# Kernel optimization log

Measured on AMD Instinct MI355X. Metric: run time of the kernel, lower is better.

The kernel has to match this reference:

```python
import jax, jax.numpy as jnp
import numpy as np

DIM = 512        # token feature dim
HID = 1024       # expert hidden dim (dim * 2)
E = 16           # num_experts
N = 8192         # num tokens
TOPK = 2         # experts active per token (routing sparsity)


def setup_inputs() -> dict:
    key = jax.random.key(0)
    k_x, k_s, k_w1, k_w2 = jax.random.split(key, 4)
    x = jax.random.normal(k_x, (N, DIM), dtype=jnp.float32)
    # sparse routing scores: top-2 experts per token get nonzero score, rest 0
    scores = jax.random.uniform(k_s, (N, E), dtype=jnp.float32)
    vals, idx = jax.lax.top_k(scores, TOPK)
    routing_tensor = jnp.zeros((N, E), jnp.float32).at[jnp.arange(N)[:, None], idx].set(vals)
    # per-expert MLP params (depth=2, bias=True): Linear(DIM->HID), GELU, Linear(HID->DIM)
    W1 = jax.random.normal(k_w1, (E, DIM, HID), dtype=jnp.float32) * (1.0 / np.sqrt(DIM))
    b1 = jnp.zeros((E, HID), jnp.float32)
    W2 = jax.random.normal(k_w2, (E, HID, DIM), dtype=jnp.float32) * (1.0 / np.sqrt(HID))
    b2 = jnp.zeros((E, DIM), jnp.float32)
    return {"x": x, "routing_tensor": routing_tensor, "W1": W1, "b1": b1, "W2": W2, "b2": b2}


def reference(x, routing_tensor, W1, b1, W2, b2):
    # out[n] = sum_e routing[n,e] * MLP_e(x[n]); rows with score 0 contribute 0,
    # which is exactly the original mask-gather / scatter-add semantics.
    h = jax.nn.gelu(jnp.einsum('nd,edh->enh', x, W1) + b1[:, None, :], approximate=False)
    y = jnp.einsum('enh,ehd->end', h, W2) + b2[:, None, :]  # [E, N, DIM]
    return jnp.einsum('end,ne->nd', y, routing_tensor)       # combine weighted by scores
```

## Files before the change

kernel.cpp:

```cpp
#include <hip/hip_runtime.h>
#include <hip/hip_bf16.h>

#define NTOK 8192
#define DIM 512
#define HID 1024
#define NE 16
#define CAP 1280
#define MT 20

typedef __attribute__((ext_vector_type(8))) short short8;
typedef __attribute__((ext_vector_type(4))) float f32x4;

static __device__ __forceinline__ unsigned short f2bf(float f) {
    __hip_bfloat16 h = __float2bfloat16(f);
    return __builtin_bit_cast(unsigned short, h);
}

static __device__ __forceinline__ void gl_lds16(const unsigned short* g, unsigned short* l) {
    __builtin_amdgcn_global_load_lds(
        (const __attribute__((address_space(1))) unsigned int*)g,
        (__attribute__((address_space(3))) unsigned int*)l, 16, 0, 0);
}

static __device__ __forceinline__ float gelu_f(float v) {
    float u = v * (0.7978845608f + 0.0356774081f * v * v);
    return v / (1.0f + __expf(-2.0f * u));
}

__global__ void transpose_cvt2(const float* __restrict__ W1, const float* __restrict__ W2,
                               unsigned short* __restrict__ w1t, unsigned short* __restrict__ w2t) {
    __shared__ float tile[32][33];
    int b = blockIdx.x;
    const float* src; unsigned short* dst; int R, C, bx, by;
    if (b < 8192) {
        int e = b >> 9, rem = b & 511; bx = rem & 31; by = rem >> 5;
        R = DIM; C = HID;
        src = W1 + (size_t)e * R * C; dst = w1t + (size_t)e * R * C;
    } else {
        int bb = b - 8192;
        int e = bb >> 9, rem = bb & 511; bx = rem & 15; by = rem >> 4;
        R = HID; C = DIM;
        src = W2 + (size_t)e * R * C; dst = w2t + (size_t)e * R * C;
    }
    int c0 = bx * 32, r0 = by * 32;
    int tx = threadIdx.x, ty = threadIdx.y;
    #pragma unroll
    for (int i = 0; i < 32; i += 8)
        tile[ty + i][tx] = src[(size_t)(r0 + ty + i) * C + c0 + tx];
    __syncthreads();
    #pragma unroll
    for (int i = 0; i < 32; i += 8)
        dst[(size_t)(c0 + ty + i) * R + r0 + tx] = f2bf(tile[tx][ty + i]);
}

__global__ __launch_bounds__(256) void route_fill(const float* __restrict__ routing,
                                                  int* __restrict__ cnt,
                                                  int* __restrict__ sidx,
                                                  float* __restrict__ wtb) {
    __shared__ int lcnt[NE], lbase[NE];
    int t = threadIdx.x;
    int n = blockIdx.x * 256 + t;
    if (t < NE) lcnt[t] = 0;
    __syncthreads();
    int mye[2]; float myw[2]; int mypos[2]; int slot = 0;
    #pragma unroll
    for (int e = 0; e < NE; e++) {
        float r = routing[n * NE + e];
        if (r != 0.0f && slot < 2) {
            mye[slot] = e; myw[slot] = r;
            mypos[slot] = atomicAdd(&lcnt[e], 1);
            slot++;
        }
    }
    __syncthreads();
    if (t < NE) lbase[t] = atomicAdd(&cnt[t], lcnt[t]);
    __syncthreads();
    for (int s = 0; s < slot; s++) {
        int e = mye[s];
        int p = lbase[e] + mypos[s];
        if (p < CAP) { sidx[e * CAP + p] = n * 2 + s; wtb[e * CAP + p] = myw[s]; }
    }
}

__global__ void gather_x(const float* __restrict__ x, const int* __restrict__ cnt,
                         const int* __restrict__ sidx, unsigned short* __restrict__ xg) {
    int b = blockIdx.x;
    int e = b / CAP, row = b - e * CAP;
    int t = threadIdx.x;
    int c = cnt[e]; c = c > CAP ? CAP : c;
    ushort4 o;
    if (row < c) {
        int n = sidx[b] >> 1;
        float4 v = ((const float4*)(x + (size_t)n * DIM))[t];
        o.x = f2bf(v.x); o.y = f2bf(v.y); o.z = f2bf(v.z); o.w = f2bf(v.w);
    } else {
        o.x = 0; o.y = 0; o.z = 0; o.w = 0;
    }
    ((ushort4*)(xg + (size_t)b * DIM))[t] = o;
}

template <int K>
__device__ __forceinline__ void mfma_main64(const unsigned short* __restrict__ A,
                                            const unsigned short* __restrict__ B,
                                            unsigned short* As, unsigned short* Bs,
                                            f32x4 acc[2][4]) {
    int t = threadIdx.x;
    int wave = t >> 6, lane = t & 63;
    int wm = wave >> 1, wn = wave & 1;
    int quad = lane >> 4, l16 = lane & 15;
    int lr = lane >> 3;
    int col = (lane & 7) << 3;
    for (int kc = 0; kc < K; kc += 64) {
        __syncthreads();
        #pragma unroll
        for (int j = 0; j < 2; j++) {
            int rb = wave * 16 + j * 8;
            gl_lds16(A + (size_t)(rb + lr) * K + kc + col, As + rb * 64);
        }
        #pragma unroll
        for (int j = 0; j < 4; j++) {
            int rb = wave * 32 + j * 8;
            gl_lds16(B + (size_t)(rb + lr) * K + kc + col, Bs + rb * 64);
        }
        __syncthreads();
        #pragma unroll
        for (int kk = 0; kk < 64; kk += 32) {
            short8 av[2], bv[4];
            #pragma unroll
            for (int mt = 0; mt < 2; mt++)
                av[mt] = *(const short8*)(&As[(wm * 32 + mt * 16 + l16) * 64 + kk + quad * 8]);
            #pragma unroll
            for (int nt = 0; nt < 4; nt++)
                bv[nt] = *(const short8*)(&Bs[(wn * 64 + nt * 16 + l16) * 64 + kk + quad * 8]);
            #pragma unroll
            for (int mt = 0; mt < 2; mt++)
                #pragma unroll
                for (int nt = 0; nt < 4; nt++)
                    acc[mt][nt] = __builtin_amdgcn_mfma_f32_16x16x32_bf16(
                        av[mt], bv[nt], acc[mt][nt], 0, 0, 0);
        }
    }
}


__global__ __launch_bounds__(256, 5) void gemm1_gelu(
    const unsigned short* __restrict__ xg, const unsigned short* __restrict__ w1t,
    const float* __restrict__ b1, const int* __restrict__ cnt,
    unsigned short* __restrict__ hbuf) {
    __shared__ __align__(16) unsigned short As[64 * 64];
    __shared__ __align__(16) unsigned short Bs[128 * 64];
    int L = blockIdx.x;
    int cc = L & 7, n = (L >> 3) & 7, g = L >> 6;
    int pi = cc + (g << 3);
    int e = pi / MT, m = pi % MT;
    int c = cnt[e]; c = c > CAP ? CAP : c;
    int m0 = m * 64;
    if (m0 >= c) return;
    int n0 = n * 128;
    const unsigned short* A = xg + ((size_t)e * CAP + m0) * DIM;
    const unsigned short* B = w1t + ((size_t)e * HID + n0) * DIM;
    f32x4 z = {0.f, 0.f, 0.f, 0.f};
    f32x4 acc[2][4];
    #pragma unroll
    for (int mt = 0; mt < 2; mt++)
        #pragma unroll
        for (int nt = 0; nt < 4; nt++) acc[mt][nt] = z;
    mfma_main64<DIM>(A, B, As, Bs, acc);
    int t = threadIdx.x;
    int wave = t >> 6, lane = t & 63;
    int wm = wave >> 1, wn = wave & 1, quad = lane >> 4, l16 = lane & 15;
    #pragma unroll
    for (int nt = 0; nt < 4; nt++) {
        int gn = n0 + wn * 64 + nt * 16 + l16;
        float bias = b1[e * HID + gn];
        #pragma unroll
        for (int mt = 0; mt < 2; mt++) {
            #pragma unroll
            for (int r = 0; r < 4; r++) {
                int gm = m0 + wm * 32 + mt * 16 + quad * 4 + r;
                float v = acc[mt][nt][r] + bias;
                hbuf[((size_t)e * CAP + gm) * HID + gn] = f2bf(gelu_f(v));
            }
        }
    }
}

__global__ __launch_bounds__(256, 5) void gemm2_store(
    const unsigned short* __restrict__ hbuf, const unsigned short* __restrict__ w2t,
    const float* __restrict__ b2, const int* __restrict__ cnt,
    const int* __restrict__ sidx, const float* __restrict__ wtb,
    float* __restrict__ ybuf) {
    __shared__ __align__(16) unsigned short As[64 * 64];
    __shared__ __align__(16) unsigned short Bs[128 * 64];
    int L = blockIdx.x;
    int cc = L & 7, n = (L >> 3) & 3, g = L >> 5;
    int pi = cc + (g << 3);
    int e = pi / MT, m = pi % MT;
    int c = cnt[e]; c = c > CAP ? CAP : c;
    int m0 = m * 64;
    if (m0 >= c) return;
    int n0 = n * 128;
    const unsigned short* A = hbuf + ((size_t)e * CAP + m0) * HID;
    const unsigned short* B = w2t + ((size_t)e * DIM + n0) * HID;
    f32x4 z = {0.f, 0.f, 0.f, 0.f};
    f32x4 acc[2][4];
    #pragma unroll
    for (int mt = 0; mt < 2; mt++)
        #pragma unroll
        for (int nt = 0; nt < 4; nt++) acc[mt][nt] = z;
    mfma_main64<HID>(A, B, As, Bs, acc);
    int t = threadIdx.x;
    int wave = t >> 6, lane = t & 63;
    int wm = wave >> 1, wn = wave & 1, quad = lane >> 4, l16 = lane & 15;
    #pragma unroll
    for (int mt = 0; mt < 2; mt++) {
        #pragma unroll
        for (int r = 0; r < 4; r++) {
            int gm = m0 + wm * 32 + mt * 16 + quad * 4 + r;
            if (gm < c) {
                int si = sidx[e * CAP + gm];
                float wgt = wtb[e * CAP + gm];
                float* yrow = ybuf + (size_t)si * DIM;
                #pragma unroll
                for (int nt = 0; nt < 4; nt++) {
                    int gn = n0 + wn * 64 + nt * 16 + l16;
                    yrow[gn] = wgt * (acc[mt][nt][r] + b2[e * DIM + gn]);
                }
            }
        }
    }
}

__global__ void combine(const float* __restrict__ yb, float* __restrict__ out) {
    int i = blockIdx.x * 256 + threadIdx.x;
    int n = i >> 7, d4 = i & 127;
    float4 a = ((const float4*)(yb + (size_t)(2 * n) * DIM))[d4];
    float4 b = ((const float4*)(yb + (size_t)(2 * n + 1) * DIM))[d4];
    float4 o;
    o.x = a.x + b.x; o.y = a.y + b.y; o.z = a.z + b.z; o.w = a.w + b.w;
    ((float4*)(out + (size_t)n * DIM))[d4] = o;
}

extern "C" void kernel_launch(void* const* d_in, const int* in_sizes, int n_in,
                              void* d_out, int out_size, void* d_ws, size_t ws_size,
                              hipStream_t stream) {
    const float* x       = (const float*)d_in[0];
    const float* routing = (const float*)d_in[1];
    const float* W1      = (const float*)d_in[2];
    const float* b1      = (const float*)d_in[3];
    const float* W2      = (const float*)d_in[4];
    const float* b2      = (const float*)d_in[5];
    float* out = (float*)d_out;

    char* w = (char*)d_ws;
    int*   cnt  = (int*)w;
    int*   sidx = (int*)(w + 256);
    float* wtb  = (float*)(w + 256 + NE * CAP * 4);
    char* base = w + 256 + NE * CAP * 8;
    unsigned short* xg  = (unsigned short*)base;
    unsigned short* hb  = xg + (size_t)NE * CAP * DIM;
    unsigned short* w1t = hb + (size_t)NE * CAP * HID;
    unsigned short* w2t = w1t + (size_t)NE * HID * DIM;
    float* ybuf = (float*)(w2t + (size_t)NE * DIM * HID);

    hipMemsetAsync(cnt, 0, 256, stream);

    transpose_cvt2<<<16384, dim3(32, 8), 0, stream>>>(W1, W2, w1t, w2t);

    route_fill<<<NTOK / 256, 256, 0, stream>>>(routing, cnt, sidx, wtb);
    gather_x<<<NE * CAP, 128, 0, stream>>>(x, cnt, sidx, xg);

    gemm1_gelu<<<8 * MT * NE, 256, 0, stream>>>(xg, w1t, b1, cnt, hb);
    gemm2_store<<<4 * MT * NE, 256, 0, stream>>>(hb, w2t, b2, cnt, sidx, wtb, ybuf);
    combine<<<(NTOK * DIM / 4) / 256, 256, 0, stream>>>(ybuf, out);
}
```

Baseline: 226.8 us.

## Merge weight transpose with routing, remap GEMM blocks so each XCD owns experts

Fuses the weight transpose/convert kernel and the routing-fill kernel into one launch, removing a kernel launch boundary. Remaps GEMM block indices so each XCD processes whole experts (expert = xcd + 8*half), so that expert's weights stay resident in that XCD's L2 cache. Raises the launch-bounds occupancy hint from 5 to 6 waves per SIMD for both GEMMs, which may force register limits or spills.

```diff
diff --git a/kernel.cpp b/kernel.cpp
--- a/kernel.cpp
+++ b/kernel.cpp
@@ -27,58 +27,61 @@
     return v / (1.0f + __expf(-2.0f * u));
 }
 
-__global__ void transpose_cvt2(const float* __restrict__ W1, const float* __restrict__ W2,
-                               unsigned short* __restrict__ w1t, unsigned short* __restrict__ w2t) {
-    __shared__ float tile[32][33];
+__global__ __launch_bounds__(256) void prep(const float* __restrict__ W1,
+                                            const float* __restrict__ W2,
+                                            unsigned short* __restrict__ w1t,
+                                            unsigned short* __restrict__ w2t,
+                                            const float* __restrict__ routing,
+                                            int* __restrict__ cnt,
+                                            int* __restrict__ sidx,
+                                            float* __restrict__ wtb) {
     int b = blockIdx.x;
-    const float* src; unsigned short* dst; int R, C, bx, by;
-    if (b < 8192) {
-        int e = b >> 9, rem = b & 511; bx = rem & 31; by = rem >> 5;
-        R = DIM; C = HID;
-        src = W1 + (size_t)e * R * C; dst = w1t + (size_t)e * R * C;
+    int t = threadIdx.x;
+    if (b < 16384) {
+        __shared__ float tile[32][33];
+        const float* src; unsigned short* dst; int R, C, bx, by;
+        if (b < 8192) {
+            int e = b >> 9, rem = b & 511; bx = rem & 31; by = rem >> 5;
+            R = DIM; C = HID;
+            src = W1 + (size_t)e * R * C; dst = w1t + (size_t)e * R * C;
+        } else {
+            int bb = b - 8192;
+            int e = bb >> 9, rem = bb & 511; bx = rem & 15; by = rem >> 4;
+            R = HID; C = DIM;
+            src = W2 + (size_t)e * R * C; dst = w2t + (size_t)e * R * C;
+        }
+        int c0 = bx * 32, r0 = by * 32;
+        int tx = t & 31, ty = t >> 5;
+        #pragma unroll
+        for (int i = 0; i < 32; i += 8)
+            tile[ty + i][tx] = src[(size_t)(r0 + ty + i) * C + c0 + tx];
+        __syncthreads();
+        #pragma unroll
+        for (int i = 0; i < 32; i += 8)
+            dst[(size_t)(c0 + ty + i) * R + r0 + tx] = f2bf(tile[tx][ty + i]);
     } else {
-        int bb = b - 8192;
-        int e = bb >> 9, rem = bb & 511; bx = rem & 15; by = rem >> 4;
-        R = HID; C = DIM;
-        src = W2 + (size_t)e * R * C; dst = w2t + (size_t)e * R * C;
-    }
-    int c0 = bx * 32, r0 = by * 32;
-    int tx = threadIdx.x, ty = threadIdx.y;
-    #pragma unroll
-    for (int i = 0; i < 32; i += 8)
-        tile[ty + i][tx] = src[(size_t)(r0 + ty + i) * C + c0 + tx];
-    __syncthreads();
-    #pragma unroll
-    for (int i = 0; i < 32; i += 8)
-        dst[(size_t)(c0 + ty + i) * R + r0 + tx] = f2bf(tile[tx][ty + i]);
-}
-
-__global__ __launch_bounds__(256) void route_fill(const float* __restrict__ routing,
-                                                  int* __restrict__ cnt,
-                                                  int* __restrict__ sidx,
-                                                  float* __restrict__ wtb) {
-    __shared__ int lcnt[NE], lbase[NE];
-    int t = threadIdx.x;
-    int n = blockIdx.x * 256 + t;
-    if (t < NE) lcnt[t] = 0;
-    __syncthreads();
-    int mye[2]; float myw[2]; int mypos[2]; int slot = 0;
-    #pragma unroll
-    for (int e = 0; e < NE; e++) {
-        float r = routing[n * NE + e];
-        if (r != 0.0f && slot < 2) {
-            mye[slot] = e; myw[slot] = r;
-            mypos[slot] = atomicAdd(&lcnt[e], 1);
-            slot++;
-        }
-    }
-    __syncthreads();
-    if (t < NE) lbase[t] = atomicAdd(&cnt[t], lcnt[t]);
-    __syncthreads();
-    for (int s = 0; s < slot; s++) {
-        int e = mye[s];
-        int p = lbase[e] + mypos[s];
-        if (p < CAP) { sidx[e * CAP + p] = n * 2 + s; wtb[e * CAP + p] = myw[s]; }
+        __shared__ int lcnt[NE], lbase[NE];
+        int n = (b - 16384) * 256 + t;
+        if (t < NE) lcnt[t] = 0;
+        __syncthreads();
+        int mye[2]; float myw[2]; int mypos[2]; int slot = 0;
+        #pragma unroll
+        for (int e = 0; e < NE; e++) {
+            float r = routing[n * NE + e];
+            if (r != 0.0f && slot < 2) {
+                mye[slot] = e; myw[slot] = r;
+                mypos[slot] = atomicAdd(&lcnt[e], 1);
+                slot++;
+            }
+        }
+        __syncthreads();
+        if (t < NE) lbase[t] = atomicAdd(&cnt[t], lcnt[t]);
+        __syncthreads();
+        for (int s = 0; s < slot; s++) {
+            int e = mye[s];
+            int p = lbase[e] + mypos[s];
+            if (p < CAP) { sidx[e * CAP + p] = n * 2 + s; wtb[e * CAP + p] = myw[s]; }
+        }
     }
 }
 
@@ -143,16 +146,18 @@
 }
 
 
-__global__ __launch_bounds__(256, 5) void gemm1_gelu(
+__global__ __launch_bounds__(256, 6) void gemm1_gelu(
     const unsigned short* __restrict__ xg, const unsigned short* __restrict__ w1t,
     const float* __restrict__ b1, const int* __restrict__ cnt,
     unsigned short* __restrict__ hbuf) {
     __shared__ __align__(16) unsigned short As[64 * 64];
     __shared__ __align__(16) unsigned short Bs[128 * 64];
     int L = blockIdx.x;
-    int cc = L & 7, n = (L >> 3) & 7, g = L >> 6;
-    int pi = cc + (g << 3);
-    int e = pi / MT, m = pi % MT;
+    int xcd = L & 7, s = L >> 3;
+    int half = (s >= 160) ? 1 : 0;
+    int t2 = s - half * 160;
+    int e = xcd + (half << 3);
+    int m = t2 >> 3, n = t2 & 7;
     int c = cnt[e]; c = c > CAP ? CAP : c;
     int m0 = m * 64;
     if (m0 >= c) return;
@@ -185,7 +190,7 @@
     }
 }
 
-__global__ __launch_bounds__(256, 5) void gemm2_store(
+__global__ __launch_bounds__(256, 6) void gemm2_store(
     const unsigned short* __restrict__ hbuf, const unsigned short* __restrict__ w2t,
     const float* __restrict__ b2, const int* __restrict__ cnt,
     const int* __restrict__ sidx, const float* __restrict__ wtb,
@@ -193,9 +198,11 @@
     __shared__ __align__(16) unsigned short As[64 * 64];
     __shared__ __align__(16) unsigned short Bs[128 * 64];
     int L = blockIdx.x;
-    int cc = L & 7, n = (L >> 3) & 3, g = L >> 5;
-    int pi = cc + (g << 3);
-    int e = pi / MT, m = pi % MT;
+    int xcd = L & 7, s = L >> 3;
+    int half = (s >= 80) ? 1 : 0;
+    int t2 = s - half * 80;
+    int e = xcd + (half << 3);
+    int m = t2 >> 2, n = t2 & 3;
     int c = cnt[e]; c = c > CAP ? CAP : c;
     int m0 = m * 64;
     if (m0 >= c) return;
@@ -265,9 +272,7 @@
 
     hipMemsetAsync(cnt, 0, 256, stream);
 
-    transpose_cvt2<<<16384, dim3(32, 8), 0, stream>>>(W1, W2, w1t, w2t);
-
-    route_fill<<<NTOK / 256, 256, 0, stream>>>(routing, cnt, sidx, wtb);
+    prep<<<16384 + NTOK / 256, 256, 0, stream>>>(W1, W2, w1t, w2t, routing, cnt, sidx, wtb);
     gather_x<<<NE * CAP, 128, 0, stream>>>(x, cnt, sidx, xg);
 
     gemm1_gelu<<<8 * MT * NE, 256, 0, stream>>>(xg, w1t, b1, cnt, hb);
```

Result: slower. 260.3 us (+14.8%).
